# Kernel tuning notes

Hardware: AMD Instinct MI355X
Metric: run time of the kernel (lower is better)

Reference implementation:

```python
import jax, jax.numpy as jnp
import numpy as np

N_NODES = 50000
N_EDGES = 500000
N_REL = 8
D = 128        # input_dim
A_DIM = 64     # attention_dim
D_OUT = 128    # output_dim


def setup_inputs() -> dict:
    key = jax.random.key(0)
    ks = jax.random.split(key, 10)
    h = jax.random.normal(ks[0], (N_NODES, D), jnp.float32)
    # relation gate tables: [R, 2*D, D]; first D rows act on dst (subject), last D on src (object)
    relations = jax.random.normal(ks[1], (N_REL, 2 * D, D), jnp.float32) * 0.05
    rel_attention = jax.random.normal(ks[2], (N_REL, A_DIM), jnp.float32) * 0.05
    W_a = jax.random.normal(ks[3], (A_DIM, 2 * D), jnp.float32) * 0.05
    b_a = jnp.zeros((A_DIM,), jnp.float32)
    W_lin = jax.random.normal(ks[4], (D_OUT, 2 * D), jnp.float32) * 0.05
    b_lin = jnp.zeros((D_OUT,), jnp.float32)
    src = jax.random.randint(ks[5], (N_EDGES,), 0, N_NODES, dtype=jnp.int32)
    dst = jax.random.randint(ks[6], (N_EDGES,), 0, N_NODES, dtype=jnp.int32)
    etype = jax.random.randint(ks[7], (N_EDGES,), 0, N_REL, dtype=jnp.int32)
    return {"h": h, "relations": relations, "rel_attention": rel_attention,
            "W_a": W_a, "b_a": b_a, "W_lin": W_lin, "b_lin": b_lin,
            "src": src, "dst": dst, "etype": etype}


def reference(h, relations, rel_attention, W_a, b_a, W_lin, b_lin, src, dst, etype):
    d = h.shape[-1]
    # --- gates: relation-indexed gather_mm (concat gate type) ---
    # Project every node through every relation once (R is small), then gather per edge.
    proj_dst = jnp.einsum('nd,rde->rne', h, relations[:, :d, :])   # [R, N, D] subject/dst side
    proj_src = jnp.einsum('nd,rde->rne', h, relations[:, d:, :])   # [R, N, D] object/src side
    gate = jax.nn.sigmoid(proj_dst[etype, dst] + proj_src[etype, src])  # [E, D]

    src_h = h[src]   # [E, D]
    dst_h = h[dst]   # [E, D]

    # --- gatv2 attention (predicates are zeroed in the module -> rel_attention[0]) ---
    a = jax.nn.leaky_relu(jnp.concatenate([dst_h, src_h], axis=-1) @ W_a.T + b_a)  # [E, A]
    score = (rel_attention[0] * a).sum(-1)  # [E]

    # --- edge_softmax over destination-node segments ---
    smax = jax.ops.segment_max(score, dst, num_segments=N_NODES)
    ex = jnp.exp(score - smax[dst])
    denom = jax.ops.segment_sum(ex, dst, num_segments=N_NODES)
    attn = ex / denom[dst]  # [E]

    # --- message = u_mul_e(h, attn*gate), reduce = sum over dst ---
    msg = src_h * (attn[:, None] * gate)                 # [E, D]
    h_N = jax.ops.segment_sum(msg, dst, num_segments=N_NODES)  # [N, D]

    # --- graphsage aggregate: LeakyReLU(W [h ; h_N] + b) ---
    out = jax.nn.leaky_relu(jnp.concatenate([h, h_N], axis=-1) @ W_lin.T + b_lin)
    return out
```

## Files before the change

### kernel.cpp

```cpp
#include <hip/hip_runtime.h>
#include <cstdint>
#include <cstddef>

constexpr int NNODES = 50000;
constexpr int NEDGES = 500000;
constexpr int NRELS  = 8;
constexpr int DIM    = 128;
constexpr int ADIM   = 64;
constexpr int TWOD   = 256;
constexpr int EPB    = 64;
constexpr float SLOPE = 0.01f;

constexpr int XPITCH = TWOD + 8;
constexpr int PPITCH = DIM + 8;

typedef __attribute__((ext_vector_type(8))) short short8;
typedef __attribute__((ext_vector_type(4))) float floatx4;

__device__ __forceinline__ unsigned short f2bf(float f) {
    unsigned u = __float_as_uint(f);
    unsigned r = u + 0x7FFFu + ((u >> 16) & 1u);
    return (unsigned short)(r >> 16);
}
__device__ __forceinline__ float bf2f(unsigned short b) {
    return __uint_as_float(((unsigned)b) << 16);
}

__device__ __forceinline__ unsigned enc_f(float f) {
    unsigned u = __float_as_uint(f);
    return (u & 0x80000000u) ? ~u : (u | 0x80000000u);
}
__device__ __forceinline__ float dec_f(unsigned k) {
    unsigned u = (k & 0x80000000u) ? (k & 0x7FFFFFFFu) : ~k;
    return __uint_as_float(u);
}

__global__ void k_init(float* __restrict__ hN, float* __restrict__ denom,
                       unsigned* __restrict__ smax_u, int* __restrict__ sorted,
                       int* __restrict__ cnts ) {
    int i = blockIdx.x * blockDim.x + threadIdx.x;
    int stride = gridDim.x * blockDim.x;
    for (int idx = i; idx < NNODES * DIM; idx += stride) hN[idx] = 0.0f;
    for (int idx = i; idx < NNODES; idx += stride) { denom[idx] = 0.0f; smax_u[idx] = 0u; }
    for (int idx = i; idx < NEDGES + 1024; idx += stride) sorted[idx] = -1;
    if (i < 16) cnts[i] = 0;
}

__global__ void k_prep(const float* __restrict__ rel, const float* __restrict__ W_lin,
                       const float* __restrict__ W_a,
                       unsigned short* __restrict__ relT, unsigned short* __restrict__ Wl,
                       unsigned short* __restrict__ Wa2) {
    int idx = blockIdx.x * 256 + threadIdx.x;
    const int NREL_ELEMS = NRELS * TWOD * DIM;
    const int WL_ELEMS = DIM * TWOD;
    const int WA2_ELEMS = DIM * DIM;
    if (idx < NREL_ELEMS) {
        int d = idx & 255;
        int o = (idx >> 8) & 127;
        int r = idx >> 15;
        relT[((size_t)r * DIM + o) * TWOD + d] = f2bf(rel[((size_t)r * TWOD + d) * DIM + o]);
    } else if (idx < NREL_ELEMS + WL_ELEMS) {
        int j = idx - NREL_ELEMS;
        Wl[j] = f2bf(W_lin[j]);
    } else if (idx < NREL_ELEMS + WL_ELEMS + WA2_ELEMS) {
        int j = idx - NREL_ELEMS - WL_ELEMS;
        int d = j & 127, o = j >> 7;
        float v = (o < ADIM) ? W_a[(size_t)o * TWOD + d] : W_a[(size_t)(o - ADIM) * TWOD + DIM + d];
        Wa2[j] = f2bf(v);
    }
}

__global__ void k_count(const int* __restrict__ ety, int* __restrict__ cnt) {
    __shared__ int hist[NRELS];
    int t = threadIdx.x;
    if (t < NRELS) hist[t] = 0;
    __syncthreads();
    int e = blockIdx.x * 256 + t;
    if (e < NEDGES) atomicAdd(&hist[ety[e]], 1);
    __syncthreads();
    if (t < NRELS && hist[t] > 0) atomicAdd(&cnt[t], hist[t]);
}

__global__ void k_prefix(const int* __restrict__ cnt, int* __restrict__ offs) {
    if (blockIdx.x == 0 && threadIdx.x == 0) {
        int off = 0;
        for (int r = 0; r < NRELS; r++) {
            offs[r] = off;
            off += ((cnt[r] + EPB - 1) / EPB) * EPB;
        }
    }
}

__global__ void k_scatter(const int* __restrict__ ety, const int* __restrict__ offs,
                          int* __restrict__ cursor, int* __restrict__ sorted) {
    __shared__ int hist[NRELS];
    __shared__ int basew[NRELS];
    int t = threadIdx.x;
    if (t < NRELS) hist[t] = 0;
    __syncthreads();
    int e = blockIdx.x * 256 + t;
    int r = -1, rank = 0;
    if (e < NEDGES) { r = ety[e]; rank = atomicAdd(&hist[r], 1); }
    __syncthreads();
    if (t < NRELS && hist[t] > 0) basew[t] = atomicAdd(&cursor[t], hist[t]);
    __syncthreads();
    if (e < NEDGES) sorted[offs[r] + basew[r] + rank] = e;
}

__global__ __launch_bounds__(256) void k_nodeproj(const float* __restrict__ h,
                                                  const unsigned short* __restrict__ Wa2,
                                                  float* __restrict__ proj) {
    __shared__ unsigned short Xs[EPB * PPITCH];
    const int t = threadIdx.x;
    const int nb = blockIdx.x * 64;

#pragma unroll
    for (int u = 0; u < 4; u++) {
        int v = u * 256 + t;
        int i = v >> 4;
        int c = v & 15;
        int n = nb + i;
        if (n >= NNODES) n = NNODES - 1;
        const float4* hp = (const float4*)(h + (size_t)n * DIM + c * 8);
        float4 a = hp[0], b = hp[1];
        union { unsigned short us[8]; short8 s8; } pk;
        pk.us[0] = f2bf(a.x); pk.us[1] = f2bf(a.y); pk.us[2] = f2bf(a.z); pk.us[3] = f2bf(a.w);
        pk.us[4] = f2bf(b.x); pk.us[5] = f2bf(b.y); pk.us[6] = f2bf(b.z); pk.us[7] = f2bf(b.w);
        *(short8*)&Xs[i * PPITCH + c * 8] = pk.s8;
    }

    const int wave = t >> 6;
    const int lane = t & 63;
    const int q = lane >> 4;
    const int l16 = lane & 15;

    short8 Bf[2][4];
#pragma unroll
    for (int nn = 0; nn < 2; nn++) {
        int o = (wave * 2 + nn) * 16 + l16;
        const unsigned short* bp = Wa2 + (size_t)o * DIM + q * 8;
#pragma unroll
        for (int ks = 0; ks < 4; ks++) Bf[nn][ks] = *(const short8*)(bp + ks * 32);
    }

    __syncthreads();

    floatx4 acc[4][2];
#pragma unroll
    for (int m = 0; m < 4; m++)
#pragma unroll
        for (int nn = 0; nn < 2; nn++) acc[m][nn] = (floatx4)(0.0f);

#pragma unroll
    for (int ks = 0; ks < 4; ks++) {
        short8 Af[4];
        const unsigned short* xb = &Xs[l16 * PPITCH + ks * 32 + q * 8];
#pragma unroll
        for (int m = 0; m < 4; m++) Af[m] = *(const short8*)(xb + m * 16 * PPITCH);
#pragma unroll
        for (int m = 0; m < 4; m++)
#pragma unroll
            for (int nn = 0; nn < 2; nn++)
                acc[m][nn] = __builtin_amdgcn_mfma_f32_16x16x32_bf16(Af[m], Bf[nn][ks], acc[m][nn], 0, 0, 0);
    }

#pragma unroll
    for (int m = 0; m < 4; m++) {
        int ib = m * 16 + q * 4;
#pragma unroll
        for (int nn = 0; nn < 2; nn++) {
            int o = (wave * 2 + nn) * 16 + l16;
#pragma unroll
            for (int rg = 0; rg < 4; rg++) {
                int n = nb + ib + rg;
                if (n < NNODES) proj[(size_t)n * DIM + o] = acc[m][nn][rg];
            }
        }
    }
}

__global__ __launch_bounds__(256) void k_score(const float* __restrict__ proj,
                                               const float* __restrict__ b_a, const float* __restrict__ ratt,
                                               const int* __restrict__ src, const int* __restrict__ dst,
                                               float* __restrict__ score, unsigned* __restrict__ smax_u) {
    int e = blockIdx.x * 4 + (threadIdx.x >> 6);
    int lane = threadIdx.x & 63;
    if (e >= NEDGES) return;
    int sn = src[e], dn = dst[e];
    float v = proj[(size_t)dn * DIM + lane] + proj[(size_t)sn * DIM + ADIM + lane] + b_a[lane];
    v = v > 0.0f ? v : SLOPE * v;
    v *= ratt[lane];
#pragma unroll
    for (int off = 32; off > 0; off >>= 1) v += __shfl_down(v, off);
    if (lane == 0) {
        score[e] = v;
        atomicMax(&smax_u[dn], enc_f(v));
    }
}

__global__ void k_expsum(const float* __restrict__ score, const int* __restrict__ dst,
                         const unsigned* __restrict__ smax_u, float* __restrict__ exv,
                         float* __restrict__ denom) {
    int e = blockIdx.x * 256 + threadIdx.x;
    if (e < NEDGES) {
        int dn = dst[e];
        float sm = dec_f(smax_u[dn]);
        float x = __expf(score[e] - sm);
        exv[e] = x;
        atomicAdd(&denom[dn], x);
    }
}

__global__ __launch_bounds__(256) void k_gate_msg(
    const float* __restrict__ h, const unsigned short* __restrict__ relT,
    const int* __restrict__ sorted, const int* __restrict__ srcA, const int* __restrict__ dstA,
    const int* __restrict__ etyA, const float* __restrict__ exA, const float* __restrict__ denomA,
    float* __restrict__ hN) {
    __shared__ unsigned short Xs[EPB * XPITCH];
    __shared__ int eid_s[EPB];
    __shared__ int dstn_s[EPB];
    __shared__ int srcn_s[EPB];
    __shared__ float att_s[EPB];
    __shared__ int r_s;

    const int t = threadIdx.x;
    const int base = blockIdx.x * EPB;

    if (t < EPB) {
        int e = sorted[base + t];
        eid_s[t] = e;
        if (e >= 0) {
            int dn = dstA[e], sn = srcA[e];
            dstn_s[t] = dn;
            srcn_s[t] = sn;
            att_s[t] = exA[e] / denomA[dn];
        } else {
            dstn_s[t] = 0;
            srcn_s[t] = 0;
            att_s[t] = 0.0f;
        }
        if (t == 0) r_s = (e >= 0) ? etyA[e] : 0;
    }
    __syncthreads();
    if (eid_s[0] < 0) return;
    const int r = r_s;

#pragma unroll
    for (int u = 0; u < 8; u++) {
        int v = u * 256 + t;
        int i = v >> 5;
        int c = v & 31;
        int node = (c < 16) ? dstn_s[i] : srcn_s[i];
        const float4* hp = (const float4*)(h + (size_t)node * DIM + (c & 15) * 8);
        float4 a = hp[0], b = hp[1];
        union { unsigned short us[8]; short8 s8; } pk;
        pk.us[0] = f2bf(a.x); pk.us[1] = f2bf(a.y); pk.us[2] = f2bf(a.z); pk.us[3] = f2bf(a.w);
        pk.us[4] = f2bf(b.x); pk.us[5] = f2bf(b.y); pk.us[6] = f2bf(b.z); pk.us[7] = f2bf(b.w);
        *(short8*)&Xs[i * XPITCH + c * 8] = pk.s8;
    }

    const int wave = t >> 6;
    const int lane = t & 63;
    const int q = lane >> 4;
    const int l16 = lane & 15;

    short8 Bf[2][8];
#pragma unroll
    for (int nn = 0; nn < 2; nn++) {
        int o = (wave * 2 + nn) * 16 + l16;
        const unsigned short* bp = relT + ((size_t)r * DIM + o) * TWOD + q * 8;
#pragma unroll
        for (int ks = 0; ks < 8; ks++) Bf[nn][ks] = *(const short8*)(bp + ks * 32);
    }

    __syncthreads();

    floatx4 acc[4][2];
#pragma unroll
    for (int m = 0; m < 4; m++)
#pragma unroll
        for (int nn = 0; nn < 2; nn++) acc[m][nn] = (floatx4)(0.0f);

#pragma unroll
    for (int ks = 0; ks < 8; ks++) {
        short8 Af[4];
        const unsigned short* xb = &Xs[l16 * XPITCH + ks * 32 + q * 8];
#pragma unroll
        for (int m = 0; m < 4; m++) Af[m] = *(const short8*)(xb + m * 16 * XPITCH);
#pragma unroll
        for (int m = 0; m < 4; m++)
#pragma unroll
            for (int nn = 0; nn < 2; nn++)
                acc[m][nn] = __builtin_amdgcn_mfma_f32_16x16x32_bf16(Af[m], Bf[nn][ks], acc[m][nn], 0, 0, 0);
    }

#pragma unroll
    for (int m = 0; m < 4; m++) {
        int ib = m * 16 + q * 4;
#pragma unroll
        for (int nn = 0; nn < 2; nn++) {
            int o = (wave * 2 + nn) * 16 + l16;
#pragma unroll
            for (int rg = 0; rg < 4; rg++) {
                int i = ib + rg;
                if (eid_s[i] < 0) continue;
                float g = 1.0f / (1.0f + __expf(-acc[m][nn][rg]));
                float sh = bf2f(Xs[i * XPITCH + DIM + o]);
                float msg = sh * att_s[i] * g;
                atomicAdd(&hN[(size_t)dstn_s[i] * DIM + o], msg);
            }
        }
    }
}

__global__ __launch_bounds__(256) void k_out(const float* __restrict__ h, const float* __restrict__ hN,
                                             const unsigned short* __restrict__ Wl,
                                             const float* __restrict__ b_lin,
                                             float* __restrict__ out) {
    __shared__ unsigned short Xs[EPB * XPITCH];
    const int t = threadIdx.x;
    const int nb = blockIdx.x * 64;

#pragma unroll
    for (int u = 0; u < 8; u++) {
        int v = u * 256 + t;
        int i = v >> 5;
        int c = v & 31;
        int n = nb + i;
        if (n >= NNODES) n = NNODES - 1;
        const float* srcp = (c < 16) ? h : hN;
        const float4* hp = (const float4*)(srcp + (size_t)n * DIM + (c & 15) * 8);
        float4 a = hp[0], b = hp[1];
        union { unsigned short us[8]; short8 s8; } pk;
        pk.us[0] = f2bf(a.x); pk.us[1] = f2bf(a.y); pk.us[2] = f2bf(a.z); pk.us[3] = f2bf(a.w);
        pk.us[4] = f2bf(b.x); pk.us[5] = f2bf(b.y); pk.us[6] = f2bf(b.z); pk.us[7] = f2bf(b.w);
        *(short8*)&Xs[i * XPITCH + c * 8] = pk.s8;
    }

    const int wave = t >> 6;
    const int lane = t & 63;
    const int q = lane >> 4;
    const int l16 = lane & 15;

    short8 Bf[2][8];
#pragma unroll
    for (int nn = 0; nn < 2; nn++) {
        int o = (wave * 2 + nn) * 16 + l16;
        const unsigned short* bp = Wl + (size_t)o * TWOD + q * 8;
#pragma unroll
        for (int ks = 0; ks < 8; ks++) Bf[nn][ks] = *(const short8*)(bp + ks * 32);
    }

    __syncthreads();

    floatx4 acc[4][2];
#pragma unroll
    for (int m = 0; m < 4; m++)
#pragma unroll
        for (int nn = 0; nn < 2; nn++) acc[m][nn] = (floatx4)(0.0f);

#pragma unroll
    for (int ks = 0; ks < 8; ks++) {
        short8 Af[4];
        const unsigned short* xb = &Xs[l16 * XPITCH + ks * 32 + q * 8];
#pragma unroll
        for (int m = 0; m < 4; m++) Af[m] = *(const short8*)(xb + m * 16 * XPITCH);
#pragma unroll
        for (int m = 0; m < 4; m++)
#pragma unroll
            for (int nn = 0; nn < 2; nn++)
                acc[m][nn] = __builtin_amdgcn_mfma_f32_16x16x32_bf16(Af[m], Bf[nn][ks], acc[m][nn], 0, 0, 0);
    }

#pragma unroll
    for (int m = 0; m < 4; m++) {
        int ib = m * 16 + q * 4;
#pragma unroll
        for (int nn = 0; nn < 2; nn++) {
            int o = (wave * 2 + nn) * 16 + l16;
            float bl = b_lin[o];
#pragma unroll
            for (int rg = 0; rg < 4; rg++) {
                int n = nb + ib + rg;
                if (n < NNODES) {
                    float val = acc[m][nn][rg] + bl;
                    val = val > 0.0f ? val : SLOPE * val;
                    out[(size_t)n * DIM + o] = val;
                }
            }
        }
    }
}

extern "C" void kernel_launch(void* const* d_in, const int* in_sizes, int n_in,
                              void* d_out, int out_size, void* d_ws, size_t ws_size,
                              hipStream_t stream) {
    const float* h     = (const float*)d_in[0];
    const float* rel   = (const float*)d_in[1];
    const float* ratt  = (const float*)d_in[2];
    const float* W_a   = (const float*)d_in[3];
    const float* b_a   = (const float*)d_in[4];
    const float* W_lin = (const float*)d_in[5];
    const float* b_lin = (const float*)d_in[6];
    const int* src = (const int*)d_in[7];
    const int* dst = (const int*)d_in[8];
    const int* ety = (const int*)d_in[9];
    float* out = (float*)d_out;

    float* wsf   = (float*)d_ws;
    float* score = wsf;
    float* exv   = score + NEDGES;
    float* denom = exv + NEDGES;
    float* proj  = denom + NNODES;
    float* hN    = proj + (size_t)NNODES * DIM;
    unsigned* smax_u = (unsigned*)(hN + (size_t)NNODES * DIM);
    int* sorted  = (int*)(smax_u + NNODES);
    int* cnts    = sorted + (NEDGES + 1024);
    int* offs    = cnts + 16;
    unsigned short* relT = (unsigned short*)(offs + 8);
    unsigned short* Wl   = relT + (size_t)NRELS * DIM * TWOD;
    unsigned short* Wa2  = Wl + (size_t)DIM * TWOD;

    k_init<<<25000, 256, 0, stream>>>(hN, denom, smax_u, sorted, cnts);
    k_prep<<<(NRELS * TWOD * DIM + DIM * TWOD + DIM * DIM + 255) / 256, 256, 0, stream>>>(
        rel, W_lin, W_a, relT, Wl, Wa2);
    k_count<<<(NEDGES + 255) / 256, 256, 0, stream>>>(ety, cnts);
    k_prefix<<<1, 64, 0, stream>>>(cnts, offs);
    k_scatter<<<(NEDGES + 255) / 256, 256, 0, stream>>>(ety, offs, cnts + 8, sorted);
    k_nodeproj<<<(NNODES + 63) / 64, 256, 0, stream>>>(h, Wa2, proj);
    k_score<<<NEDGES / 4, 256, 0, stream>>>(proj, b_a, ratt, src, dst, score, smax_u);
    k_expsum<<<(NEDGES + 255) / 256, 256, 0, stream>>>(score, dst, smax_u, exv, denom);
    k_gate_msg<<<(NEDGES + 8 * EPB + EPB - 1) / EPB, 256, 0, stream>>>(
        h, relT, sorted, src, dst, ety, exv, denom, hN);
    k_out<<<(NNODES + 63) / 64, 256, 0, stream>>>(h, hN, Wl, b_lin, out);
}
```

Measured before the change: 553.4 us.

## Replace per-edge atomic scatter with bf16 message buffer and CSR gather aggregation

Instead of atomically adding each 128-wide edge message into hN, the gate kernel writes bf16 messages to a per-edge buffer, and a new kernel sums them per destination node using a dst-sorted CSR built by histogram, scan and scatter kernels. This is meant to remove 64M float atomics to random addresses. In exchange it adds a 128MB write and read of the buffer, extra launches including a single-block scan, and rounds messages to bf16 before summation. A fallback keeps the atomic path when the workspace is too small.

```diff
diff --git a/kernel.cpp b/kernel.cpp
--- a/kernel.cpp
+++ b/kernel.cpp
@@ -13,6 +13,7 @@
 
 constexpr int XPITCH = TWOD + 8;
 constexpr int PPITCH = DIM + 8;
+constexpr int MPITCH = DIM + 8;
 
 typedef __attribute__((ext_vector_type(8))) short short8;
 typedef __attribute__((ext_vector_type(4))) float floatx4;
@@ -37,11 +38,15 @@
 
 __global__ void k_init(float* __restrict__ hN, float* __restrict__ denom,
                        unsigned* __restrict__ smax_u, int* __restrict__ sorted,
-                       int* __restrict__ cnts ) {
+                       int* __restrict__ cnts ,
+                       int* __restrict__ histD, int* __restrict__ cursorD) {
     int i = blockIdx.x * blockDim.x + threadIdx.x;
     int stride = gridDim.x * blockDim.x;
     for (int idx = i; idx < NNODES * DIM; idx += stride) hN[idx] = 0.0f;
-    for (int idx = i; idx < NNODES; idx += stride) { denom[idx] = 0.0f; smax_u[idx] = 0u; }
+    for (int idx = i; idx < NNODES; idx += stride) {
+        denom[idx] = 0.0f; smax_u[idx] = 0u;
+        if (histD) { histD[idx] = 0; cursorD[idx] = 0; }
+    }
     for (int idx = i; idx < NEDGES + 1024; idx += stride) sorted[idx] = -1;
     if (i < 16) cnts[i] = 0;
 }
@@ -107,6 +112,45 @@
     if (e < NEDGES) sorted[offs[r] + basew[r] + rank] = e;
 }
 
+__global__ void k_histD(const int* __restrict__ dst, int* __restrict__ histD) {
+    int e = blockIdx.x * 256 + threadIdx.x;
+    if (e < NEDGES) atomicAdd(&histD[dst[e]], 1);
+}
+
+__global__ __launch_bounds__(1024) void k_scanD(const int* __restrict__ histD,
+                                                int* __restrict__ row_ptr) {
+    __shared__ int ls[1024];
+    const int t = threadIdx.x;
+    const int CH = (NNODES + 1023) / 1024;
+    const int base = t * CH;
+    int s = 0;
+    for (int j = 0; j < CH; j++) { int i = base + j; if (i < NNODES) s += histD[i]; }
+    ls[t] = s;
+    __syncthreads();
+    for (int off = 1; off < 1024; off <<= 1) {
+        int v = (t >= off) ? ls[t - off] : 0;
+        __syncthreads();
+        ls[t] += v;
+        __syncthreads();
+    }
+    int run = (t == 0) ? 0 : ls[t - 1];
+    for (int j = 0; j < CH; j++) {
+        int i = base + j;
+        if (i < NNODES) { row_ptr[i] = run; run += histD[i]; }
+    }
+    if (t == 1023) row_ptr[NNODES] = ls[1023];
+}
+
+__global__ void k_dscatter(const int* __restrict__ dst, const int* __restrict__ row_ptr,
+                           int* __restrict__ cursorD, int* __restrict__ dcsr) {
+    int e = blockIdx.x * 256 + threadIdx.x;
+    if (e < NEDGES) {
+        int dn = dst[e];
+        int pos = row_ptr[dn] + atomicAdd(&cursorD[dn], 1);
+        dcsr[pos] = e;
+    }
+}
+
 __global__ __launch_bounds__(256) void k_nodeproj(const float* __restrict__ h,
                                                   const unsigned short* __restrict__ Wa2,
                                                   float* __restrict__ proj) {
@@ -215,8 +259,9 @@
     const float* __restrict__ h, const unsigned short* __restrict__ relT,
     const int* __restrict__ sorted, const int* __restrict__ srcA, const int* __restrict__ dstA,
     const int* __restrict__ etyA, const float* __restrict__ exA, const float* __restrict__ denomA,
-    float* __restrict__ hN) {
+    float* __restrict__ hN, unsigned short* __restrict__ msgbuf) {
     __shared__ unsigned short Xs[EPB * XPITCH];
+    __shared__ unsigned short Ms[EPB * MPITCH];
     __shared__ int eid_s[EPB];
     __shared__ int dstn_s[EPB];
     __shared__ int srcn_s[EPB];
@@ -294,23 +339,68 @@
                 acc[m][nn] = __builtin_amdgcn_mfma_f32_16x16x32_bf16(Af[m], Bf[nn][ks], acc[m][nn], 0, 0, 0);
     }
 
-#pragma unroll
-    for (int m = 0; m < 4; m++) {
-        int ib = m * 16 + q * 4;
-#pragma unroll
-        for (int nn = 0; nn < 2; nn++) {
-            int o = (wave * 2 + nn) * 16 + l16;
-#pragma unroll
-            for (int rg = 0; rg < 4; rg++) {
-                int i = ib + rg;
-                if (eid_s[i] < 0) continue;
-                float g = 1.0f / (1.0f + __expf(-acc[m][nn][rg]));
-                float sh = bf2f(Xs[i * XPITCH + DIM + o]);
-                float msg = sh * att_s[i] * g;
-                atomicAdd(&hN[(size_t)dstn_s[i] * DIM + o], msg);
+    if (msgbuf) {
+#pragma unroll
+        for (int m = 0; m < 4; m++) {
+            int ib = m * 16 + q * 4;
+#pragma unroll
+            for (int nn = 0; nn < 2; nn++) {
+                int o = (wave * 2 + nn) * 16 + l16;
+#pragma unroll
+                for (int rg = 0; rg < 4; rg++) {
+                    int i = ib + rg;
+                    float g = 1.0f / (1.0f + __expf(-acc[m][nn][rg]));
+                    float sh = bf2f(Xs[i * XPITCH + DIM + o]);
+                    Ms[i * MPITCH + o] = f2bf(sh * att_s[i] * g);
+                }
             }
         }
-    }
+        __syncthreads();
+#pragma unroll
+        for (int u = 0; u < 4; u++) {
+            int v = u * 256 + t;
+            int i = v >> 4;
+            int c = v & 15;
+            int e = eid_s[i];
+            if (e < 0) continue;
+            short8 val = *(const short8*)&Ms[i * MPITCH + c * 8];
+            *(short8*)&msgbuf[(size_t)e * DIM + c * 8] = val;
+        }
+    } else {
+#pragma unroll
+        for (int m = 0; m < 4; m++) {
+            int ib = m * 16 + q * 4;
+#pragma unroll
+            for (int nn = 0; nn < 2; nn++) {
+                int o = (wave * 2 + nn) * 16 + l16;
+#pragma unroll
+                for (int rg = 0; rg < 4; rg++) {
+                    int i = ib + rg;
+                    if (eid_s[i] < 0) continue;
+                    float g = 1.0f / (1.0f + __expf(-acc[m][nn][rg]));
+                    float sh = bf2f(Xs[i * XPITCH + DIM + o]);
+                    float msg = sh * att_s[i] * g;
+                    atomicAdd(&hN[(size_t)dstn_s[i] * DIM + o], msg);
+                }
+            }
+        }
+    }
+}
+
+__global__ __launch_bounds__(256) void k_aggr(const unsigned short* __restrict__ msgbuf,
+                                              const int* __restrict__ row_ptr,
+                                              const int* __restrict__ dcsr,
+                                              float* __restrict__ hN) {
+    int n = blockIdx.x * 2 + (threadIdx.x >> 7);
+    int o = threadIdx.x & 127;
+    if (n >= NNODES) return;
+    int p0 = row_ptr[n], p1 = row_ptr[n + 1];
+    float acc = 0.0f;
+    for (int p = p0; p < p1; p++) {
+        int e = dcsr[p];
+        acc += bf2f(msgbuf[(size_t)e * DIM + o]);
+    }
+    hN[(size_t)n * DIM + o] = acc;
 }
 
 __global__ __launch_bounds__(256) void k_out(const float* __restrict__ h, const float* __restrict__ hN,
@@ -420,8 +510,17 @@
     unsigned short* relT = (unsigned short*)(offs + 8);
     unsigned short* Wl   = relT + (size_t)NRELS * DIM * TWOD;
     unsigned short* Wa2  = Wl + (size_t)DIM * TWOD;
-
-    k_init<<<25000, 256, 0, stream>>>(hN, denom, smax_u, sorted, cnts);
+    int* histD   = (int*)(Wa2 + (size_t)DIM * DIM);
+    int* row_ptr = histD + NNODES;
+    int* cursorD = row_ptr + (NNODES + 1);
+    int* dcsr    = cursorD + NNODES;
+    unsigned short* msgbuf = (unsigned short*)(((uintptr_t)(dcsr + NEDGES) + 255) & ~(uintptr_t)255);
+
+    size_t need = (size_t)((char*)(msgbuf + (size_t)NEDGES * DIM) - (char*)d_ws);
+    bool pathA = (ws_size >= need);
+
+    k_init<<<25000, 256, 0, stream>>>(hN, denom, smax_u, sorted, cnts,
+                                      pathA ? histD : nullptr, pathA ? cursorD : nullptr);
     k_prep<<<(NRELS * TWOD * DIM + DIM * TWOD + DIM * DIM + 255) / 256, 256, 0, stream>>>(
         rel, W_lin, W_a, relT, Wl, Wa2);
     k_count<<<(NEDGES + 255) / 256, 256, 0, stream>>>(ety, cnts);
@@ -430,7 +529,16 @@
     k_nodeproj<<<(NNODES + 63) / 64, 256, 0, stream>>>(h, Wa2, proj);
     k_score<<<NEDGES / 4, 256, 0, stream>>>(proj, b_a, ratt, src, dst, score, smax_u);
     k_expsum<<<(NEDGES + 255) / 256, 256, 0, stream>>>(score, dst, smax_u, exv, denom);
-    k_gate_msg<<<(NEDGES + 8 * EPB + EPB - 1) / EPB, 256, 0, stream>>>(
-        h, relT, sorted, src, dst, ety, exv, denom, hN);
+    if (pathA) {
+        k_histD<<<(NEDGES + 255) / 256, 256, 0, stream>>>(dst, histD);
+        k_scanD<<<1, 1024, 0, stream>>>(histD, row_ptr);
+        k_dscatter<<<(NEDGES + 255) / 256, 256, 0, stream>>>(dst, row_ptr, cursorD, dcsr);
+        k_gate_msg<<<(NEDGES + 8 * EPB + EPB - 1) / EPB, 256, 0, stream>>>(
+            h, relT, sorted, src, dst, ety, exv, denom, hN, msgbuf);
+        k_aggr<<<(NNODES + 1) / 2, 256, 0, stream>>>(msgbuf, row_ptr, dcsr, hN);
+    } else {
+        k_gate_msg<<<(NEDGES + 8 * EPB + EPB - 1) / EPB, 256, 0, stream>>>(
+            h, relT, sorted, src, dst, ety, exv, denom, hN, nullptr);
+    }
     k_out<<<(NNODES + 63) / 64, 256, 0, stream>>>(h, hN, Wl, b_lin, out);
 }
```

After: 691.3 us. +24.9%, slower.
